# Kernel optimization log

Measured on AMD Instinct MI355X. Metric: run time of the kernel, lower is better.

Reference implementation:

```python
import jax, jax.numpy as jnp
import numpy as np
import math

S, B, D, H = 2048, 2, 1024, 16
DK = D // H

def setup_inputs() -> dict:
    key = jax.random.key(0)
    ks = jax.random.split(key, 32)
    f = lambda k, shape, s=1.0: jax.random.normal(k, shape, dtype=jnp.float32) * s
    inp = {
        'qx': f(ks[0], (S, B, D)),
        'kx': f(ks[1], (S, B, D)),
        'vx': f(ks[2], (S, B, D)),
        'qc': f(ks[3], (S, B, D)),
        'kc': f(ks[4], (S, B, D)),
    }
    w = 1.0 / math.sqrt(D)
    names = ['qx_lin', 'kx_lin', 'vx_lin', 'qc_lin', 'kc_lin', 'out_lin']
    for i, n in enumerate(names):
        inp['W_' + n] = f(ks[5 + 2 * i], (D, D), w)
        inp['b_' + n] = f(ks[6 + 2 * i], (D,), w)
    vnames = ['Vqx', 'Vqc', 'Vkx', 'Vkc']
    for i, n in enumerate(vnames):
        inp['W_' + n] = f(ks[17 + 2 * i], (D, 1), w)
        inp['b_' + n] = f(ks[18 + 2 * i], (1,), w)
    return inp

def _forward(qx, kx, vx, qc, kc,
             W_qx_lin, b_qx_lin, W_kx_lin, b_kx_lin, W_vx_lin, b_vx_lin,
             W_qc_lin, b_qc_lin, W_kc_lin, b_kc_lin, W_out_lin, b_out_lin,
             W_Vqx, b_Vqx, W_Vqc, b_Vqc, W_Vkx, b_Vkx, W_Vkc, b_Vkc):
    # [S,B,D] -> [B,S,D]
    qx = jnp.swapaxes(qx, 0, 1)
    kx = jnp.swapaxes(kx, 0, 1)
    vx = jnp.swapaxes(vx, 0, 1)
    qc = jnp.swapaxes(qc, 0, 1)
    kc = jnp.swapaxes(kc, 0, 1)
    bs = qx.shape[0]

    qx = qx @ W_qx_lin + b_qx_lin
    kx = kx @ W_kx_lin + b_kx_lin
    v = vx @ W_vx_lin + b_vx_lin
    qc = qc @ W_qc_lin + b_qc_lin
    kc = kc @ W_kc_lin + b_kc_lin

    lam_q = jax.nn.sigmoid((qx @ W_Vqx + b_Vqx) + (qc @ W_Vqc + b_Vqc))  # [B,S,1]
    lam_k = jax.nn.sigmoid((kx @ W_Vkx + b_Vkx) + (kc @ W_Vkc + b_Vkc))
    q = (1.0 - lam_q) * qx + lam_q * qc
    k = (1.0 - lam_k) * kx + lam_k * kc

    # [B,S,D] -> [B,H,S,dk]
    q = q.reshape(bs, -1, H, DK).transpose(0, 2, 1, 3)
    k = k.reshape(bs, -1, H, DK).transpose(0, 2, 1, 3)
    v = v.reshape(bs, -1, H, DK).transpose(0, 2, 1, 3)

    scores = jnp.einsum('bhqd,bhkd->bhqk', q, k) / math.sqrt(DK)
    attn = jax.nn.softmax(scores, axis=-1)  # dropout is identity in eval
    ctx = jnp.einsum('bhqk,bhkd->bhqd', attn, v)

    concat = ctx.transpose(0, 2, 1, 3).reshape(bs, -1, D)
    out = concat @ W_out_lin + b_out_lin
    return jnp.swapaxes(out, 0, 1)  # back to [S,B,D]

def reference(qx, kx, vx, qc, kc,
              W_qx_lin, b_qx_lin, W_kx_lin, b_kx_lin, W_vx_lin, b_vx_lin,
              W_qc_lin, b_qc_lin, W_kc_lin, b_kc_lin, W_out_lin, b_out_lin,
              W_Vqx, b_Vqx, W_Vqc, b_Vqc, W_Vkx, b_Vkx, W_Vkc, b_Vkc):
    return _forward(qx, kx, vx, qc, kc,
                    W_qx_lin, b_qx_lin, W_kx_lin, b_kx_lin, W_vx_lin, b_vx_lin,
                    W_qc_lin, b_qc_lin, W_kc_lin, b_kc_lin, W_out_lin, b_out_lin,
                    W_Vqx, b_Vqx, W_Vqc, b_Vqc, W_Vkx, b_Vkx, W_Vkc, b_Vkc)
```

## Files before the change

kernel.cpp:

```cpp
#include <hip/hip_runtime.h>
#include <math.h>

typedef unsigned short u16;
typedef __attribute__((ext_vector_type(8))) short short8;
typedef __attribute__((ext_vector_type(4))) float floatx4;
typedef __attribute__((ext_vector_type(4))) unsigned short ushort4v;
typedef __attribute__((ext_vector_type(2))) unsigned int uint2v;

__device__ __forceinline__ float bf2f(u16 x) {
    union { unsigned int u; float f; } v; v.u = ((unsigned int)x) << 16; return v.f;
}
__device__ __forceinline__ u16 f2bf(float f) {
    union { float f; unsigned int u; } v; v.f = f;
    unsigned int r = v.u + 0x7fffu + ((v.u >> 16) & 1u);
    return (u16)(r >> 16);
}
__device__ __forceinline__ unsigned int pk2bf(float a, float b) {
#if __has_builtin(__builtin_amdgcn_cvt_pk_bf16_f32)
    auto r = __builtin_amdgcn_cvt_pk_bf16_f32(a, b);
    union { decltype(r) v; unsigned int u; } cv; cv.v = r; return cv.u;
#else
    return (unsigned int)f2bf(a) | ((unsigned int)f2bf(b) << 16);
#endif
}

__device__ __forceinline__ void swap32(unsigned int& x0, unsigned int& x1, int lane) {
#if __has_builtin(__builtin_amdgcn_permlane32_swap)
    (void)lane;
    auto r = __builtin_amdgcn_permlane32_swap((int)x0, (int)x1, false, false);
    x0 = (unsigned int)r[0]; x1 = (unsigned int)r[1];
#else
    const bool hi = (lane & 32) != 0;
    const unsigned int s = hi ? x0 : x1;
    const unsigned int rr = (unsigned int)__shfl_xor((int)s, 32, 64);
    const unsigned int n0 = hi ? rr : x0;
    const unsigned int n1 = hi ? x1 : rr;
    x0 = n0; x1 = n1;
#endif
}
__device__ __forceinline__ void swap16(unsigned int& x0, unsigned int& x1, int lane) {
#if __has_builtin(__builtin_amdgcn_permlane16_swap)
    (void)lane;
    auto r = __builtin_amdgcn_permlane16_swap((int)x0, (int)x1, false, false);
    x0 = (unsigned int)r[0]; x1 = (unsigned int)r[1];
#else
    const bool hi = (lane & 16) != 0;
    const unsigned int s = hi ? x0 : x1;
    const unsigned int rr = (unsigned int)__shfl_xor((int)s, 16, 64);
    const unsigned int n0 = hi ? rr : x0;
    const unsigned int n1 = hi ? x1 : rr;
    x0 = n0; x1 = n1;
#endif
}

__device__ __forceinline__ void g2l16(const u16* g, u16* l) {
    __builtin_amdgcn_global_load_lds(
        (const __attribute__((address_space(1))) void*)g,
        (__attribute__((address_space(3))) void*)l, 16, 0, 0);
}

struct WFuseJobs { const float* W[4]; const float* wv[4]; const float* bl[4];
                   float* out[4]; float* bdot; };

__global__ __launch_bounds__(256) void wfuse(WFuseJobs wf) {
    const int z = blockIdx.y;
    const float* W = wf.W[z];
    const float* wv = wf.wv[z];
    float* out = wf.out[z];
    const int t = threadIdx.x;
    const int lane = t & 63, w = t >> 6;
#pragma unroll
    for (int i = 0; i < 4; i++) {
        const int row = blockIdx.x * 16 + w * 4 + i;
        const float* Wr = W + (size_t)row * 1024 + lane * 16;
        const float* vr = wv + lane * 16;
        float p = 0.f;
#pragma unroll
        for (int c = 0; c < 4; c++) {
            const floatx4 a = *(const floatx4*)(Wr + c * 4);
            const floatx4 b = *(const floatx4*)(vr + c * 4);
            p += a[0] * b[0] + a[1] * b[1] + a[2] * b[2] + a[3] * b[3];
        }
#pragma unroll
        for (int m = 1; m <= 32; m <<= 1) p += __shfl_xor(p, m);
        if (lane == 0) out[row] = p;
    }
    if (blockIdx.x == 0) {
        const floatx4 bb = *(const floatx4*)(wf.bl[z] + t * 4);
        const floatx4 vv = *(const floatx4*)(wv + t * 4);
        float p = bb[0] * vv[0] + bb[1] * vv[1] + bb[2] * vv[2] + bb[3] * vv[3];
#pragma unroll
        for (int m = 1; m <= 32; m <<= 1) p += __shfl_xor(p, m);
        __shared__ float red[4];
        if ((t & 63) == 0) red[t >> 6] = p;
        __syncthreads();
        if (t == 0) wf.bdot[z] = red[0] + red[1] + red[2] + red[3];
    }
}

struct GCJobs {
    const float* xa[3]; const float* xc[3];
    const float* w1[3]; const float* w2[3];
    const float* bdot;
    const float* sA[3]; const float* sB[3];
    float* lamout[3];
    u16* dst[3];
};

__global__ __launch_bounds__(256) void gatecast(GCJobs gj) {
    const int z = blockIdx.y;
    const int row = blockIdx.x;
    const int t = threadIdx.x;
    const size_t off = (size_t)row * 1024 + t * 4;
    const floatx4 a = *(const floatx4*)(gj.xa[z] + off);

    if (z == 2) {
        ushort4v o;
        const unsigned int lo = pk2bf(a[0], a[1]);
        const unsigned int hi = pk2bf(a[2], a[3]);
        o[0] = (u16)(lo & 0xffff); o[1] = (u16)(lo >> 16);
        o[2] = (u16)(hi & 0xffff); o[3] = (u16)(hi >> 16);
        *(ushort4v*)(gj.dst[2] + (size_t)row * 1024 + t * 4) = o;
        return;
    }

    const floatx4 c  = *(const floatx4*)(gj.xc[z] + off);
    const floatx4 w1 = *(const floatx4*)(gj.w1[z] + t * 4);
    const floatx4 w2 = *(const floatx4*)(gj.w2[z] + t * 4);
    float p = 0.f;
#pragma unroll
    for (int j = 0; j < 4; j++) p += a[j] * w1[j] + c[j] * w2[j];
#pragma unroll
    for (int m = 1; m <= 32; m <<= 1) p += __shfl_xor(p, m);
    __shared__ float red[4];
    if ((t & 63) == 0) red[t >> 6] = p;
    __syncthreads();
    const float x = red[0] + red[1] + red[2] + red[3]
                  + gj.bdot[2 * z] + gj.bdot[2 * z + 1]
                  + gj.sA[z][0] + gj.sB[z][0];
    const float lam = 1.f / (1.f + exp2f(-x * 1.44269504f));
    if (t == 0) gj.lamout[z][row] = lam;
    const float oml = 1.f - lam;

    u16* d = gj.dst[z] + (size_t)row * 2048 + t * 4;
    ushort4v o1, o2;
    {
        const unsigned int lo = pk2bf(oml * a[0], oml * a[1]);
        const unsigned int hi = pk2bf(oml * a[2], oml * a[3]);
        o1[0] = (u16)(lo & 0xffff); o1[1] = (u16)(lo >> 16);
        o1[2] = (u16)(hi & 0xffff); o1[3] = (u16)(hi >> 16);
    }
    {
        const unsigned int lo = pk2bf(lam * c[0], lam * c[1]);
        const unsigned int hi = pk2bf(lam * c[2], lam * c[3]);
        o2[0] = (u16)(lo & 0xffff); o2[1] = (u16)(lo >> 16);
        o2[2] = (u16)(hi & 0xffff); o2[3] = (u16)(hi >> 16);
    }
    *(ushort4v*)d = o1;
    *(ushort4v*)(d + 1024) = o2;
}

struct WTJobs { const float* src[6]; u16* dst[6]; int stride[6]; int koff[6]; };

__global__ __launch_bounds__(256) void wtrans(WTJobs wj) {
    __shared__ float tile[32][33];
    const int z = blockIdx.z;
    const float* W = wj.src[z];
    u16* Wt = wj.dst[z];
    const int stride = wj.stride[z], koff = wj.koff[z];
    const int n0 = blockIdx.x * 32, k0 = blockIdx.y * 32;
    const int tx = threadIdx.x & 31, ty = threadIdx.x >> 5;
#pragma unroll
    for (int i = 0; i < 4; i++)
        tile[ty + i * 8][tx] = W[(size_t)(k0 + ty + i * 8) * 1024 + n0 + tx];
    __syncthreads();
#pragma unroll
    for (int i = 0; i < 4; i++)
        Wt[(size_t)(n0 + ty + i * 8) * stride + koff + k0 + tx] = f2bf(tile[tx][ty + i * 8]);
}

__global__ __launch_bounds__(256) void vtrans(const u16* __restrict__ V,
                                              u16* __restrict__ Vtg) {
    __shared__ u16 tile[32][34];
    const int bh = blockIdx.z, b = bh >> 4, h = bh & 15;
    const int base = b * 1024 + h * 64;
    const int s0 = blockIdx.x * 32, d0 = blockIdx.y * 32;
    const int tx = threadIdx.x & 31, ty = threadIdx.x >> 5;
#pragma unroll
    for (int i = 0; i < 4; i++)
        tile[ty + i * 8][tx] = V[(size_t)(s0 + ty + i * 8) * 2048 + base + d0 + tx];
    __syncthreads();
#pragma unroll
    for (int i = 0; i < 4; i++)
        Vtg[((size_t)bh * 64 + d0 + ty + i * 8) * 2048 + s0 + tx] = tile[tx][ty + i * 8];
}

struct PJob {
    const u16* A; const u16* Bt; int K;
    const float* biasA; const float* biasC; const float* lam; u16* out;
};
struct PJobs { PJob j[3]; };

__global__ __launch_bounds__(256, 3) void projall(PJobs jobs) {
    __shared__ u16 As[128 * 32];
    __shared__ u16 Bs[128 * 32];
    const PJob jb = jobs.j[blockIdx.z];
    const int K = jb.K;
    const int m0 = blockIdx.y * 128;
    const int n0 = blockIdx.x * 128;
    const int t = threadIdx.x;
    const int lane = t & 63;
    const int wid = t >> 6;
    const int wm = wid >> 1, wn = wid & 1;
    const int qd = lane >> 4, lm = lane & 15;

    const floatx4 zero4 = {0.f, 0.f, 0.f, 0.f};
    floatx4 acc[4][4];
#pragma unroll
    for (int i = 0; i < 4; i++)
#pragma unroll
        for (int j2 = 0; j2 < 4; j2++) acc[i][j2] = zero4;

    const int srow = t >> 1, colb = (t & 1) * 16;
    const u16* Ap = jb.A + (size_t)(m0 + srow) * K + colb;
    const u16* Bp = jb.Bt + (size_t)(n0 + srow) * K + colb;
    u16* awr = &As[srow * 32 + colb];
    u16* bwr = &Bs[srow * 32 + colb];

    short8 pa0 = *(const short8*)Ap;
    short8 pa1 = *(const short8*)(Ap + 8);
    short8 pb0 = *(const short8*)Bp;
    short8 pb1 = *(const short8*)(Bp + 8);

    for (int k0 = 0; k0 < K; k0 += 32) {
        __syncthreads();
        *(short8*)awr       = pa0;
        *(short8*)(awr + 8) = pa1;
        *(short8*)bwr       = pb0;
        *(short8*)(bwr + 8) = pb1;
        if (k0 + 32 < K) {
            Ap += 32; Bp += 32;
            pa0 = *(const short8*)Ap;
            pa1 = *(const short8*)(Ap + 8);
            pb0 = *(const short8*)Bp;
            pb1 = *(const short8*)(Bp + 8);
        }
        __syncthreads();

        short8 af[4], bfg[4];
#pragma unroll
        for (int i = 0; i < 4; i++) {
            af[i]  = *(const short8*)&As[(wm * 64 + i * 16 + lm) * 32 + qd * 8];
            bfg[i] = *(const short8*)&Bs[(wn * 64 + i * 16 + lm) * 32 + qd * 8];
        }
#pragma unroll
        for (int i = 0; i < 4; i++)
#pragma unroll
            for (int j2 = 0; j2 < 4; j2++)
                acc[i][j2] = __builtin_amdgcn_mfma_f32_16x16x32_bf16(af[i], bfg[j2], acc[i][j2], 0, 0, 0);
    }

#pragma unroll
    for (int i = 0; i < 4; i++) {
        const int mb = m0 + wm * 64 + i * 16 + qd * 4;
        float lamv[4];
        if (jb.lam) {
#pragma unroll
            for (int r = 0; r < 4; r++) lamv[r] = jb.lam[mb + r];
        }
#pragma unroll
        for (int j2 = 0; j2 < 4; j2++) {
            const int col = n0 + wn * 64 + j2 * 16 + lm;
            const float bA = jb.biasA[col];
            if (jb.lam) {
                const float dB = jb.biasC[col] - bA;
#pragma unroll
                for (int r = 0; r < 4; r++)
                    jb.out[(size_t)(mb + r) * 1024 + col] = f2bf(acc[i][j2][r] + bA + lamv[r] * dB);
            } else {
#pragma unroll
                for (int r = 0; r < 4; r++)
                    jb.out[(size_t)(mb + r) * 1024 + col] = f2bf(acc[i][j2][r] + bA);
            }
        }
    }
}

__global__ __launch_bounds__(256, 4) void gemm64(const u16* __restrict__ A,
                                                 const u16* __restrict__ Bt,
                                                 const float* __restrict__ bias,
                                                 float* __restrict__ C) {
    __shared__ u16 As[64 * 32];
    __shared__ u16 Bs[128 * 32];
    const int K = 1024;
    const int m0 = blockIdx.y * 64;
    const int n0 = blockIdx.x * 128;
    const int t = threadIdx.x;
    const int lane = t & 63;
    const int wid = t >> 6;
    const int wm = wid >> 1, wn = wid & 1;
    const int qd = lane >> 4, lm = lane & 15;

    const floatx4 zero4 = {0.f, 0.f, 0.f, 0.f};
    floatx4 acc[2][4];
#pragma unroll
    for (int i = 0; i < 2; i++)
#pragma unroll
        for (int j2 = 0; j2 < 4; j2++) acc[i][j2] = zero4;

    const int ar = t >> 2, ac_ = (t & 3) * 8;
    const int br = t >> 1, bc_ = (t & 1) * 16;
    const u16* Ap = A + (size_t)(m0 + ar) * K + ac_;
    const u16* Bp = Bt + (size_t)(n0 + br) * K + bc_;
    u16* awr = &As[ar * 32 + ac_];
    u16* bwr = &Bs[br * 32 + bc_];

    short8 pa0, pb0, pb1;
    pa0 = *(const short8*)Ap;
    pb0 = *(const short8*)Bp; pb1 = *(const short8*)(Bp + 8);

    for (int k0 = 0; k0 < K; k0 += 32) {
        __syncthreads();
        *(short8*)awr = pa0;
        *(short8*)bwr = pb0;
        *(short8*)(bwr + 8) = pb1;
        if (k0 + 32 < K) {
            Ap += 32; Bp += 32;
            pa0 = *(const short8*)Ap;
            pb0 = *(const short8*)Bp; pb1 = *(const short8*)(Bp + 8);
        }
        __syncthreads();

        short8 af[2], bfg[4];
#pragma unroll
        for (int i = 0; i < 2; i++)
            af[i] = *(const short8*)&As[(wm * 32 + i * 16 + lm) * 32 + qd * 8];
#pragma unroll
        for (int j2 = 0; j2 < 4; j2++)
            bfg[j2] = *(const short8*)&Bs[(wn * 64 + j2 * 16 + lm) * 32 + qd * 8];
#pragma unroll
        for (int i = 0; i < 2; i++)
#pragma unroll
            for (int j2 = 0; j2 < 4; j2++)
                acc[i][j2] = __builtin_amdgcn_mfma_f32_16x16x32_bf16(af[i], bfg[j2], acc[i][j2], 0, 0, 0);
    }

#pragma unroll
    for (int i = 0; i < 2; i++) {
        const int mb = m0 + wm * 32 + i * 16 + qd * 4;
#pragma unroll
        for (int j2 = 0; j2 < 4; j2++) {
            const int col = n0 + wn * 64 + j2 * 16 + lm;
            const float bv = bias[col];
#pragma unroll
            for (int r = 0; r < 4; r++)
                C[(size_t)(mb + r) * 1024 + col] = acc[i][j2][r] + bv;
        }
    }
}

__global__ __launch_bounds__(256, 4) void attn5(
    const u16* __restrict__ Q, const u16* __restrict__ Kk,
    const u16* __restrict__ Vtg, float* __restrict__ ctxp,
    float* __restrict__ lp) {
    __shared__ __align__(16) u16 SB[16384];

    const int bid = blockIdx.x + 16 * (blockIdx.y + 32 * blockIdx.z);
    const int sw = (bid & 7) * 128 + (bid >> 3);
    const int qt = sw & 15;
    const int bh = (sw >> 4) & 31;
    const int sp = sw >> 9;
    const int b = bh >> 4, h = bh & 15;
    const int hb = b * 1024 + h * 64;

    const int t = threadIdx.x, lane = t & 63, w = t >> 6;
    const int qd = lane >> 4, lm = lane & 15;
    const int q0w = qt * 128 + w * 32;

    short8 qf[2][2];
#pragma unroll
    for (int qh = 0; qh < 2; qh++) {
        const u16* qr = Q + (size_t)(q0w + qh * 16 + lm) * 2048 + hb;
#pragma unroll
        for (int c = 0; c < 2; c++)
            qf[qh][c] = *(const short8*)(qr + c * 32 + qd * 8);
    }

    const floatx4 zero4 = {0.f, 0.f, 0.f, 0.f};
    floatx4 ctx[2][4];
#pragma unroll
    for (int qh = 0; qh < 2; qh++)
#pragma unroll
        for (int g = 0; g < 4; g++) ctx[qh][g] = zero4;
    float lpart[2] = {0.f, 0.f};

    const int rl = lane >> 3;
    const int cuz = (lane & 7) ^ rl;
    const u16* kp = Kk + (size_t)(sp * 1024 + w * 16 + rl) * 2048 + hb + cuz * 8;
    const u16* vp = Vtg + ((size_t)bh * 64 + w * 16 + rl) * 2048 + sp * 1024 + cuz * 8;
    u16* kd = &SB[(w * 16) * 64];
    u16* vd = &SB[4096 + (w * 16) * 64];

    const int rdA = lm * 64 + ((qd ^ (lm & 7)) << 3);
    const int rdB = rdA ^ 32;

    const float C = 0.18033688011112042f;

#define STAGE(BUF) do {                                             \
        g2l16(kp,            kd + (BUF) * 8192);                    \
        g2l16(kp + 8 * 2048, kd + (BUF) * 8192 + 8 * 64);           \
        g2l16(vp,            vd + (BUF) * 8192);                    \
        g2l16(vp + 8 * 2048, vd + (BUF) * 8192 + 8 * 64);           \
        kp += 64 * 2048; vp += 64;                                  \
    } while (0)

#define COMPUTE(BUF) do {                                                          \
        short8 pa[2][2];                                                           \
        _Pragma("unroll")                                                          \
        for (int gp = 0; gp < 2; gp++) {                                           \
            unsigned int pw[2][2][2];                                              \
            _Pragma("unroll")                                                      \
            for (int g0 = 0; g0 < 2; g0++) {                                       \
                const int g = gp * 2 + g0;                                         \
                const short8 kf0 = *(const short8*)&SB[(BUF) * 8192 + g * 1024 + rdA]; \
                const short8 kf1 = *(const short8*)&SB[(BUF) * 8192 + g * 1024 + rdB]; \
                _Pragma("unroll")                                                  \
                for (int qh = 0; qh < 2; qh++) {                                   \
                    floatx4 st = zero4;                                            \
                    st = __builtin_amdgcn_mfma_f32_16x16x32_bf16(kf0, qf[qh][0], st, 0, 0, 0); \
                    st = __builtin_amdgcn_mfma_f32_16x16x32_bf16(kf1, qf[qh][1], st, 0, 0, 0); \
                    const float e0 = exp2f(st[0] * C), e1 = exp2f(st[1] * C);      \
                    const float e2 = exp2f(st[2] * C), e3 = exp2f(st[3] * C);      \
                    lpart[qh] += (e0 + e1) + (e2 + e3);                            \
                    pw[qh][g0][0] = pk2bf(e0, e1);                                 \
                    pw[qh][g0][1] = pk2bf(e2, e3);                                 \
                }                                                                  \
            }                                                                      \
            _Pragma("unroll")                                                      \
            for (int qh = 0; qh < 2; qh++) {                                       \
                unsigned int a0 = pw[qh][0][0], b0 = pw[qh][1][0];                 \
                unsigned int a1 = pw[qh][0][1], b1 = pw[qh][1][1];                 \
                swap32(a0, b0, lane); swap32(a1, b1, lane);                        \
                swap16(a0, b0, lane); swap16(a1, b1, lane);                        \
                union { unsigned int u[4]; short8 s; } cv;                         \
                cv.u[0] = a0; cv.u[1] = a1; cv.u[2] = b0; cv.u[3] = b1;            \
                pa[qh][gp] = cv.s;                                                 \
            }                                                                      \
        }                                                                          \
        __builtin_amdgcn_s_setprio(1);                                             \
        _Pragma("unroll")                                                          \
        for (int g = 0; g < 4; g++) {                                              \
            const short8 vb0 = *(const short8*)&SB[(BUF) * 8192 + 4096 + g * 1024 + rdA]; \
            const short8 vb1 = *(const short8*)&SB[(BUF) * 8192 + 4096 + g * 1024 + rdB]; \
            _Pragma("unroll")                                                      \
            for (int qh = 0; qh < 2; qh++) {                                       \
                ctx[qh][g] = __builtin_amdgcn_mfma_f32_16x16x32_bf16(pa[qh][0], vb0, ctx[qh][g], 0, 0, 0); \
                ctx[qh][g] = __builtin_amdgcn_mfma_f32_16x16x32_bf16(pa[qh][1], vb1, ctx[qh][g], 0, 0, 0); \
            }                                                                      \
        }                                                                          \
        __builtin_amdgcn_s_setprio(0);                                             \
    } while (0)

    STAGE(0);
#pragma unroll 1
    for (int it = 0; it < 8; it++) {
        __syncthreads();
        STAGE(1);
        COMPUTE(0);
        __syncthreads();
        if (it < 7) STAGE(0);
        COMPUTE(1);
    }
#undef STAGE
#undef COMPUTE

    float* cbase = ctxp + (size_t)sp * 4194304;
#pragma unroll
    for (int qh = 0; qh < 2; qh++) {
        float l = lpart[qh];
        l += __shfl_xor(l, 16);
        l += __shfl_xor(l, 32);
        if (lane < 16)
            lp[(size_t)sp * 65536 + bh * 2048 + q0w + qh * 16 + lane] = l;
#pragma unroll
        for (int r = 0; r < 4; r++) {
            const int srow = q0w + qh * 16 + qd * 4 + r;
            float* orow = cbase + (size_t)srow * 2048 + hb;
#pragma unroll
            for (int g = 0; g < 4; g++)
                orow[g * 16 + lm] = ctx[qh][g][r];
        }
    }
}

__global__ __launch_bounds__(256) void merge(const float* __restrict__ ctxp,
                                             const float* __restrict__ lp,
                                             u16* __restrict__ out) {
    const size_t idx = ((size_t)blockIdx.x * 256 + threadIdx.x) * 4;
    const floatx4 a = *(const floatx4*)(ctxp + idx);
    const floatx4 c = *(const floatx4*)(ctxp + 4194304 + idx);
    const int srow = (int)(idx >> 11);
    const int rem = (int)(idx & 2047);
    const int bh = rem >> 6;
    const float l = lp[bh * 2048 + srow] + lp[65536 + bh * 2048 + srow];
    const float inv = 1.0f / l;
    ushort4v o;
    const unsigned int lo = pk2bf((a[0] + c[0]) * inv, (a[1] + c[1]) * inv);
    const unsigned int hi = pk2bf((a[2] + c[2]) * inv, (a[3] + c[3]) * inv);
    o[0] = (u16)(lo & 0xffff); o[1] = (u16)(lo >> 16);
    o[2] = (u16)(hi & 0xffff); o[3] = (u16)(hi >> 16);
    *(ushort4v*)(out + idx) = o;
}

extern "C" void kernel_launch(void* const* d_in, const int* in_sizes, int n_in,
                              void* d_out, int out_size, void* d_ws, size_t ws_size,
                              hipStream_t stream) {
    const float* qx = (const float*)d_in[0];
    const float* kx = (const float*)d_in[1];
    const float* vx = (const float*)d_in[2];
    const float* qc = (const float*)d_in[3];
    const float* kc = (const float*)d_in[4];
    const float* W_qx = (const float*)d_in[5];   const float* b_qx = (const float*)d_in[6];
    const float* W_kx = (const float*)d_in[7];   const float* b_kx = (const float*)d_in[8];
    const float* W_vx = (const float*)d_in[9];   const float* b_vx = (const float*)d_in[10];
    const float* W_qc = (const float*)d_in[11];  const float* b_qc = (const float*)d_in[12];
    const float* W_kc = (const float*)d_in[13];  const float* b_kc = (const float*)d_in[14];
    const float* W_out = (const float*)d_in[15]; const float* b_out = (const float*)d_in[16];
    const float* W_Vqx = (const float*)d_in[17]; const float* b_Vqx = (const float*)d_in[18];
    const float* W_Vqc = (const float*)d_in[19]; const float* b_Vqc = (const float*)d_in[20];
    const float* W_Vkx = (const float*)d_in[21]; const float* b_Vkx = (const float*)d_in[22];
    const float* W_Vkc = (const float*)d_in[23]; const float* b_Vkc = (const float*)d_in[24];

    char* ws = (char*)d_ws;
    const size_t MB = 1048576;
    u16* Aq  = (u16*)ws;
    u16* Ak  = (u16*)(ws + 16 * MB);
    u16* Av  = (u16*)(ws + 32 * MB);
    u16* Wtq = (u16*)(ws + 40 * MB);
    u16* Wtk = (u16*)(ws + 44 * MB);
    u16* Wtv = (u16*)(ws + 48 * MB);
    u16* Wto = (u16*)(ws + 50 * MB);
    u16* Pv    = (u16*)(ws + 52 * MB);
    u16* qg    = (u16*)(ws + 60 * MB);
    u16* kg    = (u16*)(ws + 68 * MB);
    u16* ctxbf = (u16*)(ws + 76 * MB);
    float* wfused = (float*)(ws + 84 * MB);
    float* bdot   = (float*)(ws + 84 * MB + 16384);
    float* lam    = (float*)(ws + 84 * MB + 16384 + 256);
    float* l_part = (float*)(ws + 84 * MB + 16384 + 256 + 32768);
    float* ctxp = (float*)ws;
    u16* Vtg    = (u16*)(ws + 32 * MB);

    WFuseJobs wf;
    wf.W[0] = W_qx; wf.wv[0] = W_Vqx; wf.bl[0] = b_qx; wf.out[0] = wfused;
    wf.W[1] = W_qc; wf.wv[1] = W_Vqc; wf.bl[1] = b_qc; wf.out[1] = wfused + 1024;
    wf.W[2] = W_kx; wf.wv[2] = W_Vkx; wf.bl[2] = b_kx; wf.out[2] = wfused + 2048;
    wf.W[3] = W_kc; wf.wv[3] = W_Vkc; wf.bl[3] = b_kc; wf.out[3] = wfused + 3072;
    wf.bdot = bdot;
    wfuse<<<dim3(64, 4), 256, 0, stream>>>(wf);

    GCJobs gj;
    gj.xa[0] = qx; gj.xc[0] = qc; gj.w1[0] = wfused;        gj.w2[0] = wfused + 1024;
    gj.sA[0] = b_Vqx; gj.sB[0] = b_Vqc; gj.lamout[0] = lam;        gj.dst[0] = Aq;
    gj.xa[1] = kx; gj.xc[1] = kc; gj.w1[1] = wfused + 2048; gj.w2[1] = wfused + 3072;
    gj.sA[1] = b_Vkx; gj.sB[1] = b_Vkc; gj.lamout[1] = lam + 4096; gj.dst[1] = Ak;
    gj.xa[2] = vx; gj.xc[2] = nullptr; gj.w1[2] = nullptr; gj.w2[2] = nullptr;
    gj.sA[2] = nullptr; gj.sB[2] = nullptr; gj.lamout[2] = nullptr; gj.dst[2] = Av;
    gj.bdot = bdot;
    gatecast<<<dim3(4096, 3), 256, 0, stream>>>(gj);

    WTJobs wj;
    wj.src[0] = W_qx; wj.dst[0] = Wtq; wj.stride[0] = 2048; wj.koff[0] = 0;
    wj.src[1] = W_qc; wj.dst[1] = Wtq; wj.stride[1] = 2048; wj.koff[1] = 1024;
    wj.src[2] = W_kx; wj.dst[2] = Wtk; wj.stride[2] = 2048; wj.koff[2] = 0;
    wj.src[3] = W_kc; wj.dst[3] = Wtk; wj.stride[3] = 2048; wj.koff[3] = 1024;
    wj.src[4] = W_vx; wj.dst[4] = Wtv; wj.stride[4] = 1024; wj.koff[4] = 0;
    wj.src[5] = W_out; wj.dst[5] = Wto; wj.stride[5] = 1024; wj.koff[5] = 0;
    wtrans<<<dim3(32, 32, 6), 256, 0, stream>>>(wj);

    PJobs pj;
    pj.j[0].A = Aq; pj.j[0].Bt = Wtq; pj.j[0].K = 2048;
    pj.j[0].biasA = b_qx; pj.j[0].biasC = b_qc; pj.j[0].lam = lam;        pj.j[0].out = qg;
    pj.j[1].A = Ak; pj.j[1].Bt = Wtk; pj.j[1].K = 2048;
    pj.j[1].biasA = b_kx; pj.j[1].biasC = b_kc; pj.j[1].lam = lam + 4096; pj.j[1].out = kg;
    pj.j[2].A = Av; pj.j[2].Bt = Wtv; pj.j[2].K = 1024;
    pj.j[2].biasA = b_vx; pj.j[2].biasC = nullptr; pj.j[2].lam = nullptr; pj.j[2].out = Pv;
    projall<<<dim3(8, 32, 3), 256, 0, stream>>>(pj);

    vtrans<<<dim3(64, 2, 32), 256, 0, stream>>>(Pv, Vtg);

    attn5<<<dim3(16, 32, 2), 256, 0, stream>>>(qg, kg, Vtg, ctxp, l_part);

    merge<<<4096, 256, 0, stream>>>(ctxp, l_part, ctxbf);

    gemm64<<<dim3(8, 64), 256, 0, stream>>>(ctxbf, Wto, b_out, (float*)d_out);
}
```

Baseline: 343.7 us.

## Double-buffer projection GEMM with async loads, fold softmax scale into Q, MFMA row sums

The projection GEMM now uses double-buffered LDS filled by direct global-to-LDS loads (g2l16), with one barrier per K step instead of two, and register staging is removed. The same kernel replaces the separate output GEMM by writing fp32 through a new outf path. The softmax exponent scale is folded into Q at projection time, so attention calls the raw exp2 builtin without a multiply. Attention row sums are now taken by extra MFMAs against a ones vector rather than scalar adds and shuffles. This trades more LDS per block and extra MFMA work, plus bf16 rounding of P in the denominator, for less VALU work and better load/compute overlap.

```diff
diff --git a/kernel.cpp b/kernel.cpp
--- a/kernel.cpp
+++ b/kernel.cpp
@@ -21,6 +21,13 @@
     union { decltype(r) v; unsigned int u; } cv; cv.v = r; return cv.u;
 #else
     return (unsigned int)f2bf(a) | ((unsigned int)f2bf(b) << 16);
+#endif
+}
+__device__ __forceinline__ float fexp2(float x) {
+#if __has_builtin(__builtin_amdgcn_exp2f)
+    return __builtin_amdgcn_exp2f(x);
+#else
+    return exp2f(x);
 #endif
 }
 
@@ -197,13 +204,14 @@
 
 struct PJob {
     const u16* A; const u16* Bt; int K;
-    const float* biasA; const float* biasC; const float* lam; u16* out;
+    const float* biasA; const float* biasC; const float* lam;
+    u16* out; float* outf; float scale;
 };
-struct PJobs { PJob j[3]; };
+struct PJobs { PJob j[4]; };
 
 __global__ __launch_bounds__(256, 3) void projall(PJobs jobs) {
-    __shared__ u16 As[128 * 32];
-    __shared__ u16 Bs[128 * 32];
+    __shared__ __align__(16) u16 As[2][128 * 32];
+    __shared__ __align__(16) u16 Bs[2][128 * 32];
     const PJob jb = jobs.j[blockIdx.z];
     const int K = jb.K;
     const int m0 = blockIdx.y * 128;
@@ -221,44 +229,38 @@
 #pragma unroll
         for (int j2 = 0; j2 < 4; j2++) acc[i][j2] = zero4;
 
-    const int srow = t >> 1, colb = (t & 1) * 16;
-    const u16* Ap = jb.A + (size_t)(m0 + srow) * K + colb;
-    const u16* Bp = jb.Bt + (size_t)(n0 + srow) * K + colb;
-    u16* awr = &As[srow * 32 + colb];
-    u16* bwr = &Bs[srow * 32 + colb];
-
-    short8 pa0 = *(const short8*)Ap;
-    short8 pa1 = *(const short8*)(Ap + 8);
-    short8 pb0 = *(const short8*)Bp;
-    short8 pb1 = *(const short8*)(Bp + 8);
-
+    const u16* Ap = jb.A + (size_t)(m0 + (t >> 2)) * K + (t & 3) * 8;
+    const u16* Bp = jb.Bt + (size_t)(n0 + (t >> 2)) * K + (t & 3) * 8;
+
+#define PSTAGE(BUF, KOFF) do {                                         \
+        g2l16(Ap + (KOFF),                   &As[BUF][t * 8]);         \
+        g2l16(Ap + (KOFF) + (size_t)64 * K,  &As[BUF][2048 + t * 8]);  \
+        g2l16(Bp + (KOFF),                   &Bs[BUF][t * 8]);         \
+        g2l16(Bp + (KOFF) + (size_t)64 * K,  &Bs[BUF][2048 + t * 8]);  \
+    } while (0)
+
+    PSTAGE(0, 0);
+    __syncthreads();
+    int cur = 0;
     for (int k0 = 0; k0 < K; k0 += 32) {
-        __syncthreads();
-        *(short8*)awr       = pa0;
-        *(short8*)(awr + 8) = pa1;
-        *(short8*)bwr       = pb0;
-        *(short8*)(bwr + 8) = pb1;
-        if (k0 + 32 < K) {
-            Ap += 32; Bp += 32;
-            pa0 = *(const short8*)Ap;
-            pa1 = *(const short8*)(Ap + 8);
-            pb0 = *(const short8*)Bp;
-            pb1 = *(const short8*)(Bp + 8);
-        }
-        __syncthreads();
+        if (k0 + 32 < K) PSTAGE(cur ^ 1, k0 + 32);
 
         short8 af[4], bfg[4];
 #pragma unroll
         for (int i = 0; i < 4; i++) {
-            af[i]  = *(const short8*)&As[(wm * 64 + i * 16 + lm) * 32 + qd * 8];
-            bfg[i] = *(const short8*)&Bs[(wn * 64 + i * 16 + lm) * 32 + qd * 8];
+            af[i]  = *(const short8*)&As[cur][(wm * 64 + i * 16 + lm) * 32 + qd * 8];
+            bfg[i] = *(const short8*)&Bs[cur][(wn * 64 + i * 16 + lm) * 32 + qd * 8];
         }
 #pragma unroll
         for (int i = 0; i < 4; i++)
 #pragma unroll
             for (int j2 = 0; j2 < 4; j2++)
                 acc[i][j2] = __builtin_amdgcn_mfma_f32_16x16x32_bf16(af[i], bfg[j2], acc[i][j2], 0, 0, 0);
-    }
+
+        __syncthreads();
+        cur ^= 1;
+    }
+#undef PSTAGE
 
 #pragma unroll
     for (int i = 0; i < 4; i++) {
@@ -272,94 +274,27 @@
         for (int j2 = 0; j2 < 4; j2++) {
             const int col = n0 + wn * 64 + j2 * 16 + lm;
             const float bA = jb.biasA[col];
-            if (jb.lam) {
+            if (jb.outf) {
+#pragma unroll
+                for (int r = 0; r < 4; r++)
+                    jb.outf[(size_t)(mb + r) * 1024 + col] = acc[i][j2][r] + bA;
+            } else if (jb.lam) {
                 const float dB = jb.biasC[col] - bA;
 #pragma unroll
                 for (int r = 0; r < 4; r++)
-                    jb.out[(size_t)(mb + r) * 1024 + col] = f2bf(acc[i][j2][r] + bA + lamv[r] * dB);
+                    jb.out[(size_t)(mb + r) * 1024 + col] =
+                        f2bf((acc[i][j2][r] + bA + lamv[r] * dB) * jb.scale);
             } else {
 #pragma unroll
                 for (int r = 0; r < 4; r++)
-                    jb.out[(size_t)(mb + r) * 1024 + col] = f2bf(acc[i][j2][r] + bA);
+                    jb.out[(size_t)(mb + r) * 1024 + col] =
+                        f2bf((acc[i][j2][r] + bA) * jb.scale);
             }
         }
     }
 }
 
-__global__ __launch_bounds__(256, 4) void gemm64(const u16* __restrict__ A,
-                                                 const u16* __restrict__ Bt,
-                                                 const float* __restrict__ bias,
-                                                 float* __restrict__ C) {
-    __shared__ u16 As[64 * 32];
-    __shared__ u16 Bs[128 * 32];
-    const int K = 1024;
-    const int m0 = blockIdx.y * 64;
-    const int n0 = blockIdx.x * 128;
-    const int t = threadIdx.x;
-    const int lane = t & 63;
-    const int wid = t >> 6;
-    const int wm = wid >> 1, wn = wid & 1;
-    const int qd = lane >> 4, lm = lane & 15;
-
-    const floatx4 zero4 = {0.f, 0.f, 0.f, 0.f};
-    floatx4 acc[2][4];
-#pragma unroll
-    for (int i = 0; i < 2; i++)
-#pragma unroll
-        for (int j2 = 0; j2 < 4; j2++) acc[i][j2] = zero4;
-
-    const int ar = t >> 2, ac_ = (t & 3) * 8;
-    const int br = t >> 1, bc_ = (t & 1) * 16;
-    const u16* Ap = A + (size_t)(m0 + ar) * K + ac_;
-    const u16* Bp = Bt + (size_t)(n0 + br) * K + bc_;
-    u16* awr = &As[ar * 32 + ac_];
-    u16* bwr = &Bs[br * 32 + bc_];
-
-    short8 pa0, pb0, pb1;
-    pa0 = *(const short8*)Ap;
-    pb0 = *(const short8*)Bp; pb1 = *(const short8*)(Bp + 8);
-
-    for (int k0 = 0; k0 < K; k0 += 32) {
-        __syncthreads();
-        *(short8*)awr = pa0;
-        *(short8*)bwr = pb0;
-        *(short8*)(bwr + 8) = pb1;
-        if (k0 + 32 < K) {
-            Ap += 32; Bp += 32;
-            pa0 = *(const short8*)Ap;
-            pb0 = *(const short8*)Bp; pb1 = *(const short8*)(Bp + 8);
-        }
-        __syncthreads();
-
-        short8 af[2], bfg[4];
-#pragma unroll
-        for (int i = 0; i < 2; i++)
-            af[i] = *(const short8*)&As[(wm * 32 + i * 16 + lm) * 32 + qd * 8];
-#pragma unroll
-        for (int j2 = 0; j2 < 4; j2++)
-            bfg[j2] = *(const short8*)&Bs[(wn * 64 + j2 * 16 + lm) * 32 + qd * 8];
-#pragma unroll
-        for (int i = 0; i < 2; i++)
-#pragma unroll
-            for (int j2 = 0; j2 < 4; j2++)
-                acc[i][j2] = __builtin_amdgcn_mfma_f32_16x16x32_bf16(af[i], bfg[j2], acc[i][j2], 0, 0, 0);
-    }
-
-#pragma unroll
-    for (int i = 0; i < 2; i++) {
-        const int mb = m0 + wm * 32 + i * 16 + qd * 4;
-#pragma unroll
-        for (int j2 = 0; j2 < 4; j2++) {
-            const int col = n0 + wn * 64 + j2 * 16 + lm;
-            const float bv = bias[col];
-#pragma unroll
-            for (int r = 0; r < 4; r++)
-                C[(size_t)(mb + r) * 1024 + col] = acc[i][j2][r] + bv;
-        }
-    }
-}
-
-__global__ __launch_bounds__(256, 4) void attn5(
+__global__ __launch_bounds__(256, 4) void attn6(
     const u16* __restrict__ Q, const u16* __restrict__ Kk,
     const u16* __restrict__ Vtg, float* __restrict__ ctxp,
     float* __restrict__ lp) {
@@ -392,7 +327,11 @@
     for (int qh = 0; qh < 2; qh++)
 #pragma unroll
         for (int g = 0; g < 4; g++) ctx[qh][g] = zero4;
-    float lpart[2] = {0.f, 0.f};
+    floatx4 accL[2] = {zero4, zero4};
+
+    union { unsigned int u[4]; short8 s; } ov;
+    ov.u[0] = ov.u[1] = ov.u[2] = ov.u[3] = 0x3F803F80u;
+    const short8 onesb = ov.s;
 
     const int rl = lane >> 3;
     const int cuz = (lane & 7) ^ rl;
@@ -403,8 +342,6 @@
 
     const int rdA = lm * 64 + ((qd ^ (lm & 7)) << 3);
     const int rdB = rdA ^ 32;
-
-    const float C = 0.18033688011112042f;
 
 #define STAGE(BUF) do {                                             \
         g2l16(kp,            kd + (BUF) * 8192);                    \
@@ -429,9 +366,8 @@
                     floatx4 st = zero4;                                            \
                     st = __builtin_amdgcn_mfma_f32_16x16x32_bf16(kf0, qf[qh][0], st, 0, 0, 0); \
                     st = __builtin_amdgcn_mfma_f32_16x16x32_bf16(kf1, qf[qh][1], st, 0, 0, 0); \
-                    const float e0 = exp2f(st[0] * C), e1 = exp2f(st[1] * C);      \
-                    const float e2 = exp2f(st[2] * C), e3 = exp2f(st[3] * C);      \
-                    lpart[qh] += (e0 + e1) + (e2 + e3);                            \
+                    const float e0 = fexp2(st[0]), e1 = fexp2(st[1]);              \
+                    const float e2 = fexp2(st[2]), e3 = fexp2(st[3]);              \
                     pw[qh][g0][0] = pk2bf(e0, e1);                                 \
                     pw[qh][g0][1] = pk2bf(e2, e3);                                 \
                 }                                                                  \
@@ -458,6 +394,11 @@
                 ctx[qh][g] = __builtin_amdgcn_mfma_f32_16x16x32_bf16(pa[qh][1], vb1, ctx[qh][g], 0, 0, 0); \
             }                                                                      \
         }                                                                          \
+        _Pragma("unroll")                                                          \
+        for (int qh = 0; qh < 2; qh++) {                                           \
+            accL[qh] = __builtin_amdgcn_mfma_f32_16x16x32_bf16(pa[qh][0], onesb, accL[qh], 0, 0, 0); \
+            accL[qh] = __builtin_amdgcn_mfma_f32_16x16x32_bf16(pa[qh][1], onesb, accL[qh], 0, 0, 0); \
+        }                                                                          \
         __builtin_amdgcn_s_setprio(0);                                             \
     } while (0)
 
@@ -477,11 +418,11 @@
     float* cbase = ctxp + (size_t)sp * 4194304;
 #pragma unroll
     for (int qh = 0; qh < 2; qh++) {
-        float l = lpart[qh];
-        l += __shfl_xor(l, 16);
-        l += __shfl_xor(l, 32);
-        if (lane < 16)
-            lp[(size_t)sp * 65536 + bh * 2048 + q0w + qh * 16 + lane] = l;
+        if (lm == 0) {
+#pragma unroll
+            for (int r = 0; r < 4; r++)
+                lp[(size_t)sp * 65536 + bh * 2048 + q0w + qh * 16 + qd * 4 + r] = accL[qh][r];
+        }
 #pragma unroll
         for (int r = 0; r < 4; r++) {
             const int srow = q0w + qh * 16 + qd * 4 + r;
@@ -578,20 +519,30 @@
     wj.src[5] = W_out; wj.dst[5] = Wto; wj.stride[5] = 1024; wj.koff[5] = 0;
     wtrans<<<dim3(32, 32, 6), 256, 0, stream>>>(wj);
 
+    const float QSCALE = 0.18033688011112042f;
     PJobs pj;
     pj.j[0].A = Aq; pj.j[0].Bt = Wtq; pj.j[0].K = 2048;
-    pj.j[0].biasA = b_qx; pj.j[0].biasC = b_qc; pj.j[0].lam = lam;        pj.j[0].out = qg;
+    pj.j[0].biasA = b_qx; pj.j[0].biasC = b_qc; pj.j[0].lam = lam;
+    pj.j[0].out = qg; pj.j[0].outf = nullptr; pj.j[0].scale = QSCALE;
     pj.j[1].A = Ak; pj.j[1].Bt = Wtk; pj.j[1].K = 2048;
-    pj.j[1].biasA = b_kx; pj.j[1].biasC = b_kc; pj.j[1].lam = lam + 4096; pj.j[1].out = kg;
+    pj.j[1].biasA = b_kx; pj.j[1].biasC = b_kc; pj.j[1].lam = lam + 4096;
+    pj.j[1].out = kg; pj.j[1].outf = nullptr; pj.j[1].scale = 1.0f;
     pj.j[2].A = Av; pj.j[2].Bt = Wtv; pj.j[2].K = 1024;
-    pj.j[2].biasA = b_vx; pj.j[2].biasC = nullptr; pj.j[2].lam = nullptr; pj.j[2].out = Pv;
+    pj.j[2].biasA = b_vx; pj.j[2].biasC = nullptr; pj.j[2].lam = nullptr;
+    pj.j[2].out = Pv; pj.j[2].outf = nullptr; pj.j[2].scale = 1.0f;
+    pj.j[3] = pj.j[2];
     projall<<<dim3(8, 32, 3), 256, 0, stream>>>(pj);
 
     vtrans<<<dim3(64, 2, 32), 256, 0, stream>>>(Pv, Vtg);
 
-    attn5<<<dim3(16, 32, 2), 256, 0, stream>>>(qg, kg, Vtg, ctxp, l_part);
+    attn6<<<dim3(16, 32, 2), 256, 0, stream>>>(qg, kg, Vtg, ctxp, l_part);
 
     merge<<<4096, 256, 0, stream>>>(ctxp, l_part, ctxbf);
 
-    gemm64<<<dim3(8, 64), 256, 0, stream>>>(ctxbf, Wto, b_out, (float*)d_out);
-}
+    PJobs po;
+    po.j[0].A = ctxbf; po.j[0].Bt = Wto; po.j[0].K = 1024;
+    po.j[0].biasA = b_out; po.j[0].biasC = nullptr; po.j[0].lam = nullptr;
+    po.j[0].out = nullptr; po.j[0].outf = (float*)d_out; po.j[0].scale = 1.0f;
+    po.j[1] = po.j[0]; po.j[2] = po.j[0]; po.j[3] = po.j[0];
+    projall<<<dim3(8, 32, 1), 256, 0, stream>>>(po);
+}
```

Measured after the change: 330.9 us. -3.7%, faster.
